# Kernel tuning notes

Measured on AMD Instinct MI355X. Metric: run time of the kernel, lower is better.

## Reference

```python
import jax, jax.numpy as jnp
import numpy as np

N_NODES = 150000
N_EDGES = 2400000


def setup_inputs() -> dict:
    key = jax.random.key(0)
    ks = jax.random.split(key, 7)
    x = jax.random.normal(ks[0], (N_NODES, 9), dtype=jnp.float32)
    edge_index = jax.random.randint(ks[1], (2, N_EDGES), 0, N_NODES, dtype=jnp.int32)
    edge_weight = jax.random.uniform(ks[2], (N_EDGES,), dtype=jnp.float32, minval=0.1, maxval=1.0)
    W1 = jax.random.normal(ks[3], (9, 32), dtype=jnp.float32) * (1.0 / np.sqrt(9))
    b1 = jnp.zeros((32,), dtype=jnp.float32)
    W2 = jax.random.normal(ks[4], (32, 7), dtype=jnp.float32) * (1.0 / np.sqrt(32))
    b2 = jnp.zeros((7,), dtype=jnp.float32)
    return {"x": x, "edge_index": edge_index, "edge_weight": edge_weight,
            "W1": W1, "b1": b1, "W2": W2, "b2": b2}


def gcn_norm(edge_index, edge_weight, num_nodes):
    # PyG gcn_norm: add self-loops (weight 1), symmetric D^-1/2 A D^-1/2
    row, col = edge_index[0], edge_index[1]
    loop = jnp.arange(num_nodes, dtype=edge_index.dtype)
    row = jnp.concatenate([row, loop])
    col = jnp.concatenate([col, loop])
    w = jnp.concatenate([edge_weight, jnp.ones((num_nodes,), edge_weight.dtype)])
    deg = jax.ops.segment_sum(w, col, num_segments=num_nodes)  # [N]
    dinv = jnp.where(deg > 0, jax.lax.rsqrt(deg), 0.0)
    norm = dinv[row] * w * dinv[col]  # [E+N]
    return row, col, norm


def gcn_conv(x, W, b, row, col, norm, num_nodes):
    h = x @ W                                   # [N, out]
    msg = norm[:, None] * h[row]                # [E+N, out] gather + scale
    out = jax.ops.segment_sum(msg, col, num_segments=num_nodes)  # scatter-add
    return out + b


def reference(x, edge_index, edge_weight, W1, b1, W2, b2):
    n = x.shape[0]
    row, col, norm = gcn_norm(edge_index, edge_weight, n)
    h = jax.nn.relu(gcn_conv(x, W1, b1, row, col, norm, n))
    # dropout is identity in eval mode
    h = gcn_conv(h, W2, b2, row, col, norm, n)
    return jax.nn.log_softmax(h, axis=1)
```

## Files before the change

kernel.cpp:

```cpp
#include <hip/hip_runtime.h>
#include <hip/hip_fp16.h>

constexpr int F_IN  = 9;
constexpr int F_HID = 32;
constexpr int F_OUT = 7;

constexpr int NBKT   = 586;
constexpr int BCAP   = 4864;
constexpr int CHUNK  = 4096;

__device__ __forceinline__ int nt_load_int(const int* p) {
    return __builtin_nontemporal_load(p);
}
__device__ __forceinline__ unsigned pack_h2(float a, float b) {
    return (unsigned)__half_as_ushort(__float2half(a)) |
           ((unsigned)__half_as_ushort(__float2half(b)) << 16);
}
__device__ __forceinline__ float2 unpack_h2(unsigned u) {
    return make_float2(__half2float(__ushort_as_half((unsigned short)(u & 0xffffu))),
                       __half2float(__ushort_as_half((unsigned short)(u >> 16))));
}

__global__ __launch_bounds__(1024) void k_hist(
    const int* __restrict__ col, int* __restrict__ ghist, int E)
{
    __shared__ int h[NBKT];
    const int tid = threadIdx.x;
    for (int i = tid; i < NBKT; i += 1024) h[i] = 0;
    __syncthreads();
    const int t0 = blockIdx.x * CHUNK;
    const int kend = min(CHUNK, E - t0);
    for (int k = tid; k < kend; k += 1024)
        atomicAdd(&h[col[t0 + k] >> 8], 1);
    __syncthreads();
    int* g = ghist + (size_t)blockIdx.x * NBKT;
    for (int i = tid; i < NBKT; i += 1024) g[i] = h[i];
}

__global__ __launch_bounds__(256) void k_scan(
    int* __restrict__ ghist, int* __restrict__ cnt, int nchunk)
{
    __shared__ int sc[256];
    const int b = blockIdx.x, tid = threadIdx.x;
    const int per = (nchunk + 255) / 256;
    const int i0 = tid * per, i1 = min(i0 + per, nchunk);

    int sum = 0;
    for (int i = i0; i < i1; ++i) sum += ghist[(size_t)i * NBKT + b];
    sc[tid] = sum; __syncthreads();
    for (int d = 1; d < 256; d <<= 1) {
        int u = (tid >= d) ? sc[tid - d] : 0;
        __syncthreads();
        sc[tid] += u; __syncthreads();
    }
    int run = sc[tid] - sum;
    for (int i = i0; i < i1; ++i) {
        int v = ghist[(size_t)i * NBKT + b];
        ghist[(size_t)i * NBKT + b] = run;
        run += v;
    }
    if (tid == 255) cnt[b] = run;
}

__global__ __launch_bounds__(1024) void k_scat(
    const int* __restrict__ row, const int* __restrict__ col,
    const float* __restrict__ w, const int* __restrict__ ghist,
    int2* __restrict__ irec, int E)
{
    __shared__ int sbase[NBKT];
    __shared__ int scur[NBKT];
    const int tid = threadIdx.x;
    const int* g = ghist + (size_t)blockIdx.x * NBKT;
    for (int i = tid; i < NBKT; i += 1024) { sbase[i] = g[i]; scur[i] = 0; }
    __syncthreads();
    const int t0 = blockIdx.x * CHUNK;
    const int kend = min(CHUNK, E - t0);
    for (int k = tid; k < kend; k += 1024) {
        int e = t0 + k;
        int c = col[e];
        int b = c >> 8;
        int wq = min((int)(w[e] * 16384.0f + 0.5f), 16383);
        int rk = atomicAdd(&scur[b], 1);
        int pos = b * BCAP + sbase[b] + rk;
        if (pos < (b + 1) * BCAP)
            irec[pos] = make_int2((row[e] << 14) | wq, c & 255);
    }
}

__global__ __launch_bounds__(1024) void k_sortbucket(
    const int2* __restrict__ irec, int* __restrict__ csr4,
    const int* __restrict__ cnt, const float* __restrict__ x,
    int4* __restrict__ meta, unsigned* __restrict__ xdh, int N)
{
    __shared__ int           srw[BCAP];
    __shared__ unsigned char scb[BCAP];
    __shared__ int   hist[256];
    __shared__ float wsum[256];
    __shared__ int   nbase[256];
    __shared__ int   scur[256];

    const int b    = blockIdx.x;
    const int tid  = threadIdx.x;
    const int base = b * BCAP;
    const int c_n  = min(cnt[b], BCAP);

    if (tid < 256) { hist[tid] = 0; wsum[tid] = 0.0f; scur[tid] = 0; }
    __syncthreads();

    for (int k = tid; k < c_n; k += 1024) {
        int2 rc = irec[base + k];
        srw[k] = rc.x;
        unsigned char c = (unsigned char)(rc.y & 255);
        scb[k] = c;
        atomicAdd(&hist[c], 1);
        atomicAdd(&wsum[c], (float)(rc.x & 16383) * (1.0f / 16384.0f));
    }
    __syncthreads();

    int v = 0;
    if (tid < 256) { v = hist[tid]; nbase[tid] = v; }
    __syncthreads();
    for (int d = 1; d < 256; d <<= 1) {
        int u = (tid >= d && tid < 256) ? nbase[tid - d] : 0;
        __syncthreads();
        if (tid < 256) nbase[tid] += u;
        __syncthreads();
    }
    if (tid < 256) {
        int excl = nbase[tid] - v;
        __syncthreads();
        nbase[tid] = excl;
    } else {
        __syncthreads();
    }

    if (tid < 256) {
        int node = b * 256 + tid;
        if (node < N) {
            float dv = rsqrtf(1.0f + wsum[tid]);
            meta[node] = make_int4(base + nbase[tid], v, __float_as_int(dv), 0);
            float xv[F_IN];
            #pragma unroll
            for (int j = 0; j < F_IN; ++j) xv[j] = dv * x[(size_t)node * F_IN + j];
            size_t o = (size_t)node * 6;
            xdh[o + 0] = pack_h2(xv[0], xv[1]);
            xdh[o + 1] = pack_h2(xv[2], xv[3]);
            xdh[o + 2] = pack_h2(xv[4], xv[5]);
            xdh[o + 3] = pack_h2(xv[6], xv[7]);
            xdh[o + 4] = pack_h2(xv[8], 0.0f);
            xdh[o + 5] = 0u;
        }
    }
    __syncthreads();

    for (int k = tid; k < c_n; k += 1024) {
        int rw = srw[k];
        unsigned char c = scb[k];
        int r = atomicAdd(&scur[c], 1);
        csr4[base + nbase[c] + r] = rw;
    }
}

__global__ __launch_bounds__(256) void k_g1mlp(
    const int* __restrict__ csr4, const int4* __restrict__ meta,
    const unsigned* __restrict__ xdh,
    const float* __restrict__ W1, const float* __restrict__ b1,
    const float* __restrict__ W2, unsigned* __restrict__ h2dh, int N)
{
    __shared__ float sW1[F_IN * F_HID];
    __shared__ float sb1[F_HID];
    __shared__ float sW2[F_HID * F_OUT];
    for (int t = threadIdx.x; t < F_IN * F_HID; t += 256) sW1[t] = W1[t];
    for (int t = threadIdx.x; t < F_HID;        t += 256) sb1[t] = b1[t];
    for (int t = threadIdx.x; t < F_HID * F_OUT; t += 256) sW2[t] = W2[t];
    __syncthreads();

    int t   = blockIdx.x * 256 + threadIdx.x;
    int i   = t >> 2;
    int sub = t & 3;
    if (i >= N) return;
    int4 m = meta[i];
    float dv = __int_as_float(m.z);

    float acc[F_IN];
    #pragma unroll
    for (int j = 0; j < F_IN; ++j) acc[j] = 0.0f;
    if (sub == 0) {
        size_t o = (size_t)i * 6;
        uint2 u01 = *reinterpret_cast<const uint2*>(xdh + o);
        uint2 u23 = *reinterpret_cast<const uint2*>(xdh + o + 2);
        unsigned u4 = xdh[o + 4];
        float2 f0 = unpack_h2(u01.x), f1 = unpack_h2(u01.y),
               f2 = unpack_h2(u23.x), f3 = unpack_h2(u23.y),
               f4 = unpack_h2(u4);
        acc[0] = f0.x; acc[1] = f0.y; acc[2] = f1.x; acc[3] = f1.y;
        acc[4] = f2.x; acc[5] = f2.y; acc[6] = f3.x; acc[7] = f3.y;
        acc[8] = f4.x;
    }
    int s = m.x, tend = m.x + m.y;
    for (int e = s + sub; e < tend; e += 4) {
        int v = nt_load_int(&csr4[e]);
        int r = (int)((unsigned)v >> 14);
        float wv = (float)(v & 16383) * (1.0f / 16384.0f);
        size_t o = (size_t)r * 6;
        uint2 u01 = *reinterpret_cast<const uint2*>(xdh + o);
        uint2 u23 = *reinterpret_cast<const uint2*>(xdh + o + 2);
        unsigned u4 = xdh[o + 4];
        float2 f0 = unpack_h2(u01.x), f1 = unpack_h2(u01.y),
               f2 = unpack_h2(u23.x), f3 = unpack_h2(u23.y),
               f4 = unpack_h2(u4);
        acc[0] = fmaf(wv, f0.x, acc[0]); acc[1] = fmaf(wv, f0.y, acc[1]);
        acc[2] = fmaf(wv, f1.x, acc[2]); acc[3] = fmaf(wv, f1.y, acc[3]);
        acc[4] = fmaf(wv, f2.x, acc[4]); acc[5] = fmaf(wv, f2.y, acc[5]);
        acc[6] = fmaf(wv, f3.x, acc[6]); acc[7] = fmaf(wv, f3.y, acc[7]);
        acc[8] = fmaf(wv, f4.x, acc[8]);
    }
    #pragma unroll
    for (int d = 1; d < 4; d <<= 1) {
        #pragma unroll
        for (int j = 0; j < F_IN; ++j)
            acc[j] += __shfl_xor(acc[j], d, 4);
    }
    #pragma unroll
    for (int j = 0; j < F_IN; ++j) acc[j] *= dv;

    float o7[F_OUT];
    #pragma unroll
    for (int c = 0; c < F_OUT; ++c) o7[c] = 0.0f;
    int ks = sub * 8;
    #pragma unroll
    for (int k = 0; k < 8; ++k) {
        float hk = sb1[ks + k];
        #pragma unroll
        for (int j = 0; j < F_IN; ++j) hk = fmaf(acc[j], sW1[j * F_HID + ks + k], hk);
        hk = fmaxf(hk, 0.0f);
        #pragma unroll
        for (int c = 0; c < F_OUT; ++c) o7[c] = fmaf(hk, sW2[(ks + k) * F_OUT + c], o7[c]);
    }
    #pragma unroll
    for (int d = 1; d < 4; d <<= 1) {
        #pragma unroll
        for (int c = 0; c < F_OUT; ++c)
            o7[c] += __shfl_xor(o7[c], d, 4);
    }
    float pa = dv * o7[2 * sub];
    float pb = (2 * sub + 1 < F_OUT) ? dv * o7[2 * sub + 1] : 0.0f;
    h2dh[(size_t)i * 4 + sub] = pack_h2(pa, pb);
}

__global__ __launch_bounds__(256) void k_g2ls(
    const int* __restrict__ csr4, const int4* __restrict__ meta,
    const unsigned* __restrict__ h2dh, const float* __restrict__ b2,
    float* __restrict__ out, int N)
{
    int t   = blockIdx.x * 256 + threadIdx.x;
    int i   = t >> 2;
    int sub = t & 3;
    if (i >= N) return;
    int4 m = meta[i];
    float dv = __int_as_float(m.z);

    float acc[F_OUT];
    #pragma unroll
    for (int c = 0; c < F_OUT; ++c) acc[c] = 0.0f;
    if (sub == 0) {
        uint4 h4 = *reinterpret_cast<const uint4*>(h2dh + (size_t)i * 4);
        float2 f0 = unpack_h2(h4.x), f1 = unpack_h2(h4.y),
               f2 = unpack_h2(h4.z), f3 = unpack_h2(h4.w);
        acc[0] = f0.x; acc[1] = f0.y; acc[2] = f1.x; acc[3] = f1.y;
        acc[4] = f2.x; acc[5] = f2.y; acc[6] = f3.x;
    }
    int s = m.x, tend = m.x + m.y;
    for (int e = s + sub; e < tend; e += 4) {
        int v = nt_load_int(&csr4[e]);
        int r = (int)((unsigned)v >> 14);
        float wv = (float)(v & 16383) * (1.0f / 16384.0f);
        uint4 h4 = *reinterpret_cast<const uint4*>(h2dh + (size_t)r * 4);
        float2 f0 = unpack_h2(h4.x), f1 = unpack_h2(h4.y),
               f2 = unpack_h2(h4.z), f3 = unpack_h2(h4.w);
        acc[0] = fmaf(wv, f0.x, acc[0]); acc[1] = fmaf(wv, f0.y, acc[1]);
        acc[2] = fmaf(wv, f1.x, acc[2]); acc[3] = fmaf(wv, f1.y, acc[3]);
        acc[4] = fmaf(wv, f2.x, acc[4]); acc[5] = fmaf(wv, f2.y, acc[5]);
        acc[6] = fmaf(wv, f3.x, acc[6]);
    }
    #pragma unroll
    for (int d = 1; d < 4; d <<= 1) {
        #pragma unroll
        for (int c = 0; c < F_OUT; ++c)
            acc[c] += __shfl_xor(acc[c], d, 4);
    }

    float vv[F_OUT];
    float mx = -1e30f;
    #pragma unroll
    for (int c = 0; c < F_OUT; ++c) {
        vv[c] = dv * acc[c] + b2[c];
        mx = fmaxf(mx, vv[c]);
    }
    float ss = 0.0f;
    #pragma unroll
    for (int c = 0; c < F_OUT; ++c) ss += __expf(vv[c] - mx);
    float ls = __logf(ss);
    for (int c = sub; c < F_OUT; c += 4)
        out[(size_t)i * F_OUT + c] = vv[c] - mx - ls;
}

extern "C" void kernel_launch(void* const* d_in, const int* in_sizes, int n_in,
                              void* d_out, int out_size, void* d_ws, size_t ws_size,
                              hipStream_t stream) {
    const float* x  = (const float*)d_in[0];
    const int*   ei = (const int*)  d_in[1];
    const float* ew = (const float*)d_in[2];
    const float* W1 = (const float*)d_in[3];
    const float* b1 = (const float*)d_in[4];
    const float* W2 = (const float*)d_in[5];
    const float* b2 = (const float*)d_in[6];
    float* out = (float*)d_out;

    const int N = in_sizes[0] / F_IN;
    const int E = in_sizes[2];
    const int* row = ei;
    const int* col = ei + E;
    const int nchunk = (E + CHUNK - 1) / CHUNK;

    char* p = (char*)d_ws;
    int2*     irec  = (int2*)p;      p += sizeof(int2) * (size_t)NBKT * BCAP;
    int*      csr4  = (int*)p;       p += sizeof(int)  * (size_t)NBKT * BCAP;
    int4*     meta  = (int4*)p;      p += sizeof(int4) * (size_t)N;
    unsigned* xdh   = (unsigned*)p;  p += sizeof(unsigned) * (size_t)N * 6;
    unsigned* h2dh  = (unsigned*)p;  p += sizeof(unsigned) * (size_t)N * 4;
    int*      ghist = (int*)p;       p += sizeof(int) * (size_t)nchunk * NBKT;
    int*      cnt   = (int*)p;       p += sizeof(int) * NBKT;

    const int gN4 = (4 * N + 255) / 256;

    k_hist      <<<nchunk, 1024, 0, stream>>>(col, ghist, E);
    k_scan      <<<NBKT, 256, 0, stream>>>(ghist, cnt, nchunk);
    k_scat      <<<nchunk, 1024, 0, stream>>>(row, col, ew, ghist, irec, E);
    k_sortbucket<<<NBKT, 1024, 0, stream>>>(irec, csr4, cnt, x, meta, xdh, N);
    k_g1mlp     <<<gN4, 256, 0, stream>>>(csr4, meta, xdh, W1, b1, W2, h2dh, N);
    k_g2ls      <<<gN4, 256, 0, stream>>>(csr4, meta, h2dh, b2, out, N);
}
```

Before: 133.8 us.

## Locally sort scatter chunk in LDS and split edge records into SoA

```diff
diff --git a/kernel.cpp b/kernel.cpp
--- a/kernel.cpp
+++ b/kernel.cpp
@@ -8,6 +8,7 @@
 constexpr int NBKT   = 586;
 constexpr int BCAP   = 4864;
 constexpr int CHUNK  = 4096;
+constexpr int EPT    = CHUNK / 1024;
 
 __device__ __forceinline__ int nt_load_int(const int* p) {
     return __builtin_nontemporal_load(p);
@@ -65,32 +66,69 @@
 __global__ __launch_bounds__(1024) void k_scat(
     const int* __restrict__ row, const int* __restrict__ col,
     const float* __restrict__ w, const int* __restrict__ ghist,
-    int2* __restrict__ irec, int E)
-{
+    int* __restrict__ irA, unsigned char* __restrict__ irB, int E)
+{
+    __shared__ int           sRW[CHUNK];
+    __shared__ int           sDst[CHUNK];
+    __shared__ unsigned char sCL[CHUNK];
+    __shared__ int hist[NBKT];
+    __shared__ int lcur[NBKT];
     __shared__ int sbase[NBKT];
-    __shared__ int scur[NBKT];
+    __shared__ int sc[1024];
+
     const int tid = threadIdx.x;
     const int* g = ghist + (size_t)blockIdx.x * NBKT;
-    for (int i = tid; i < NBKT; i += 1024) { sbase[i] = g[i]; scur[i] = 0; }
-    __syncthreads();
+    for (int i = tid; i < NBKT; i += 1024) { sbase[i] = g[i]; hist[i] = 0; lcur[i] = 0; }
+    __syncthreads();
+
     const int t0 = blockIdx.x * CHUNK;
     const int kend = min(CHUNK, E - t0);
+
+    int rRW[EPT], rBC[EPT], nr = 0;
     for (int k = tid; k < kend; k += 1024) {
         int e = t0 + k;
         int c = col[e];
+        int wq = min((int)(w[e] * 16384.0f + 0.5f), 16383);
+        rRW[nr] = (row[e] << 14) | wq;
+        rBC[nr] = c;
+        atomicAdd(&hist[c >> 8], 1);
+        ++nr;
+    }
+    __syncthreads();
+
+    int v = (tid < NBKT) ? hist[tid] : 0;
+    sc[tid] = v; __syncthreads();
+    for (int d = 1; d < 1024; d <<= 1) {
+        int u = (tid >= d) ? sc[tid - d] : 0;
+        __syncthreads();
+        sc[tid] += u; __syncthreads();
+    }
+    if (tid < NBKT) hist[tid] = sc[tid] - v;
+    __syncthreads();
+
+    for (int q = 0; q < nr; ++q) {
+        int c = rBC[q];
         int b = c >> 8;
-        int wq = min((int)(w[e] * 16384.0f + 0.5f), 16383);
-        int rk = atomicAdd(&scur[b], 1);
-        int pos = b * BCAP + sbase[b] + rk;
-        if (pos < (b + 1) * BCAP)
-            irec[pos] = make_int2((row[e] << 14) | wq, c & 255);
+        int rank = atomicAdd(&lcur[b], 1);
+        int p = hist[b] + rank;
+        sRW[p] = rRW[q];
+        sCL[p] = (unsigned char)(c & 255);
+        int gp = sbase[b] + rank;
+        sDst[p] = (gp < BCAP) ? (b * BCAP + gp) : -1;
+    }
+    __syncthreads();
+
+    for (int p = tid; p < kend; p += 1024) {
+        int d = sDst[p];
+        if (d >= 0) { irA[d] = sRW[p]; irB[d] = sCL[p]; }
     }
 }
 
 __global__ __launch_bounds__(1024) void k_sortbucket(
-    const int2* __restrict__ irec, int* __restrict__ csr4,
-    const int* __restrict__ cnt, const float* __restrict__ x,
-    int4* __restrict__ meta, unsigned* __restrict__ xdh, int N)
+    const int* __restrict__ irA, const unsigned char* __restrict__ irB,
+    int* __restrict__ csr4, const int* __restrict__ cnt,
+    const float* __restrict__ x, int4* __restrict__ meta,
+    unsigned* __restrict__ xdh, int N)
 {
     __shared__ int           srw[BCAP];
     __shared__ unsigned char scb[BCAP];
@@ -108,12 +146,12 @@
     __syncthreads();
 
     for (int k = tid; k < c_n; k += 1024) {
-        int2 rc = irec[base + k];
-        srw[k] = rc.x;
-        unsigned char c = (unsigned char)(rc.y & 255);
+        int rw = irA[base + k];
+        unsigned char c = irB[base + k];
+        srw[k] = rw;
         scb[k] = c;
         atomicAdd(&hist[c], 1);
-        atomicAdd(&wsum[c], (float)(rc.x & 16383) * (1.0f / 16384.0f));
+        atomicAdd(&wsum[c], (float)(rw & 16383) * (1.0f / 16384.0f));
     }
     __syncthreads();
 
@@ -324,20 +362,21 @@
     const int nchunk = (E + CHUNK - 1) / CHUNK;
 
     char* p = (char*)d_ws;
-    int2*     irec  = (int2*)p;      p += sizeof(int2) * (size_t)NBKT * BCAP;
+    int4*     meta  = (int4*)p;      p += sizeof(int4) * (size_t)N;
+    int*      irA   = (int*)p;       p += sizeof(int)  * (size_t)NBKT * BCAP;
     int*      csr4  = (int*)p;       p += sizeof(int)  * (size_t)NBKT * BCAP;
-    int4*     meta  = (int4*)p;      p += sizeof(int4) * (size_t)N;
     unsigned* xdh   = (unsigned*)p;  p += sizeof(unsigned) * (size_t)N * 6;
     unsigned* h2dh  = (unsigned*)p;  p += sizeof(unsigned) * (size_t)N * 4;
     int*      ghist = (int*)p;       p += sizeof(int) * (size_t)nchunk * NBKT;
     int*      cnt   = (int*)p;       p += sizeof(int) * NBKT;
+    unsigned char* irB = (unsigned char*)p;
 
     const int gN4 = (4 * N + 255) / 256;
 
     k_hist      <<<nchunk, 1024, 0, stream>>>(col, ghist, E);
     k_scan      <<<NBKT, 256, 0, stream>>>(ghist, cnt, nchunk);
-    k_scat      <<<nchunk, 1024, 0, stream>>>(row, col, ew, ghist, irec, E);
-    k_sortbucket<<<NBKT, 1024, 0, stream>>>(irec, csr4, cnt, x, meta, xdh, N);
+    k_scat      <<<nchunk, 1024, 0, stream>>>(row, col, ew, ghist, irA, irB, E);
+    k_sortbucket<<<NBKT, 1024, 0, stream>>>(irA, irB, csr4, cnt, x, meta, xdh, N);
     k_g1mlp     <<<gN4, 256, 0, stream>>>(csr4, meta, xdh, W1, b1, W2, h2dh, N);
     k_g2ls      <<<gN4, 256, 0, stream>>>(csr4, meta, h2dh, b2, out, N);
 }
```

Result: faster. 131.1 us (-2.1%).
